# Performance work log

Hardware: AMD Instinct MI355X
Metric: run time of the kernel (lower is better)

Reference implementation:

```python
import jax, jax.numpy as jnp
import numpy as np

N_QUBITS = 16
NUM_CLASSES = 16
C64 = jnp.complex64


def rx_mat(theta):
    # RX(theta) = [[cos(t/2), -i sin(t/2)], [-i sin(t/2), cos(t/2)]]
    c = jnp.cos(theta / 2).astype(C64)
    s = jnp.sin(theta / 2).astype(C64)
    row0 = jnp.stack([c, -1j * s], axis=-1)
    row1 = jnp.stack([-1j * s, c], axis=-1)
    return jnp.stack([row0, row1], axis=-2)  # (..., 2, 2)


def rot_mat(phi, theta, omega):
    # PennyLane Rot = RZ(omega) RY(theta) RZ(phi)
    c = jnp.cos(theta / 2).astype(C64)
    s = jnp.sin(theta / 2).astype(C64)
    phi = phi.astype(C64)
    omega = omega.astype(C64)
    e_m = jnp.exp(-0.5j * (phi + omega))
    e_p = jnp.exp(0.5j * (phi + omega))
    e_d = jnp.exp(0.5j * (phi - omega))
    e_dm = jnp.exp(-0.5j * (phi - omega))
    return jnp.array([[e_m * c, -e_d * s], [e_dm * s, e_p * c]], dtype=C64)


def apply_1q(state, U, w):
    # state: (B, 2, ..., 2) with qubit w at axis 1+w; U: (2,2) or (B,2,2)
    s = jnp.moveaxis(state, 1 + w, -1)
    if U.ndim == 3:
        s = jnp.einsum('b...i,bji->b...j', s, U)
    else:
        s = jnp.einsum('...i,ji->...j', s, U)
    return jnp.moveaxis(s, -1, 1 + w)


def apply_crx(state, theta, ctrl, tgt):
    U = rx_mat(theta)  # (2, 2)
    s = jnp.moveaxis(state, (1 + ctrl, 1 + tgt), (-2, -1))
    s1 = jnp.einsum('...i,ji->...j', s[..., 1, :], U)
    s = jnp.stack([s[..., 0, :], s1], axis=-2)
    return jnp.moveaxis(s, (-2, -1), (1 + ctrl, 1 + tgt))


def circuit(feats, rot1, crx1, rot2, crx2):
    # feats: (B, 16) rotation angles (data re-uploading)
    B = feats.shape[0]
    state = jnp.zeros((B,) + (2,) * N_QUBITS, dtype=C64)
    state = state.at[(slice(None),) + (0,) * N_QUBITS].set(1.0)

    def layer(state, rot_w, crx_w):
        for i in range(N_QUBITS):
            state = apply_1q(state, rx_mat(feats[:, i]), i)  # batched RX
        for i in range(N_QUBITS):
            state = apply_1q(state, rot_mat(rot_w[i, 0], rot_w[i, 1], rot_w[i, 2]), i)
        for i in range(N_QUBITS):
            state = apply_crx(state, crx_w[i], i, (i + 1) % N_QUBITS)
        return state

    state = layer(state, rot1, crx1)
    state = layer(state, rot2, crx2)

    probs = (state.real ** 2 + state.imag ** 2)  # (B, 2, ..., 2) float32
    evs = []
    for i in range(N_QUBITS):
        p = jnp.moveaxis(probs, 1 + i, 1).reshape(B, 2, -1).sum(-1)
        evs.append(p[:, 0] - p[:, 1])  # <Z_i>
    return jnp.stack(evs, axis=1)  # (B, 16)


def adaptive_pool_441(x):
    # AdaptiveAvgPool3d((4,4,1)) with divisible dims -> block means
    B, C, D, H, W = x.shape
    x = x.reshape(B, C, 4, D // 4, 4, H // 4, 1, W)
    return x.mean(axis=(3, 5, 7))  # (B, C, 4, 4, 1)


def setup_inputs() -> dict:
    key = jax.random.key(0)
    ks = jax.random.split(key, 9)
    B = 128
    x = jax.random.normal(ks[0], (B, 2, 16, 64, 64), dtype=jnp.float32)
    compress_w = jax.random.normal(ks[1], (N_QUBITS, 32), jnp.float32) * 0.1
    compress_b = jax.random.normal(ks[2], (N_QUBITS,), jnp.float32) * 0.01
    rot1 = jax.random.normal(ks[3], (N_QUBITS, 3), jnp.float32) * 0.1
    crx1 = jax.random.normal(ks[4], (N_QUBITS,), jnp.float32) * 0.1
    rot2 = jax.random.normal(ks[5], (N_QUBITS, 3), jnp.float32) * 0.1
    crx2 = jax.random.normal(ks[6], (N_QUBITS,), jnp.float32) * 0.1
    fc_w = jax.random.normal(ks[7], (NUM_CLASSES, N_QUBITS), jnp.float32) * 0.1
    fc_b = jax.random.normal(ks[8], (NUM_CLASSES,), jnp.float32) * 0.01
    return {"x": x, "compress_w": compress_w, "compress_b": compress_b,
            "rot1": rot1, "crx1": crx1, "rot2": rot2, "crx2": crx2,
            "fc_w": fc_w, "fc_b": fc_b}


def reference(x, compress_w, compress_b, rot1, crx1, rot2, crx2, fc_w, fc_b):
    B = x.shape[0]
    p = adaptive_pool_441(x).reshape(B, -1)          # (B, 32)
    feats = p @ compress_w.T + compress_b            # (B, 16)
    q_out = circuit(feats, rot1, crx1, rot2, crx2)   # (B, 16)
    logits = q_out @ fc_w.T + fc_b                   # (B, 16)
    return jax.nn.log_softmax(logits, axis=1)
```

## Files before the change

### kernel.cpp

```cpp
#include <hip/hip_runtime.h>
#include <hip/hip_bf16.h>

typedef float f2 __attribute__((ext_vector_type(2)));

__device__ __forceinline__ f2 sgate(f2 a, int lane, int kt, int kc, const float* u) {
    f2 p;
    p.x = __shfl_xor(a.x, 1 << kt);
    p.y = __shfl_xor(a.y, 1 << kt);
    const float* uu = u + ((kc >= 0 && ((lane >> kc) & 1)) ? 8 : 0);
    int bit = (lane >> kt) & 1;
    float cAr = bit ? uu[6] : uu[0], cAi = bit ? uu[7] : uu[1];
    float cPr = bit ? uu[4] : uu[2], cPi = bit ? uu[5] : uu[3];
    f2 r;
    r.x = cAr * a.x - cAi * a.y + cPr * p.x - cPi * p.y;
    r.y = cAr * a.y + cAi * a.x + cPr * p.y + cPi * p.x;
    return r;
}

__device__ __forceinline__ f2 cmul(f2 A, f2 B) {
    return f2{A.x * B.x - A.y * B.y, A.x * B.y + A.y * B.x};
}
__device__ __forceinline__ f2 cmulc(f2 x, f2 y) {
    return f2{x.x * y.x + x.y * y.y, x.y * y.x - x.x * y.y};
}

__global__ __launch_bounds__(256) void qall2(const float* __restrict__ x,
                                             const float* __restrict__ cw,
                                             const float* __restrict__ cb,
                                             const float* __restrict__ rot1,
                                             const float* __restrict__ crx1,
                                             const float* __restrict__ rot2,
                                             const float* __restrict__ crx2,
                                             const float* __restrict__ fcw,
                                             const float* __restrict__ fcb,
                                             float* __restrict__ out) {
    __shared__ float pp[32];
    __shared__ float uM[32][16];
    __shared__ float cs15[4];
    __shared__ f2 ell[64];
    __shared__ f2 Rr[2][64];
    __shared__ f2 Wl[2][32];
    __shared__ f2 Btab[4][64];
    __shared__ f2 Ctab[8][32];
    __shared__ float Rtab[2][4][64];
    __shared__ float sH[2][6][32];
    __shared__ float sD[2][32];
    __shared__ float sE[2][32];
    __shared__ float redP[4][7];
    __shared__ float redQ[4][8];
    __shared__ float evf[16];
    __shared__ float lgf[16];
    int tid = threadIdx.x;
    int b = blockIdx.x;

    {
        int g = tid >> 3, sub = tid & 7;
        int c = g >> 4, dd = (g >> 2) & 3, hh = g & 3;
        const float4* xb = (const float4*)(x + (size_t)b * 131072)
                         + c * 16384 + dd * 4096 + hh * 256;
        float sum = 0.f;
        #pragma unroll
        for (int d = 0; d < 4; ++d) {
            const float4* ch = xb + d * 1024;
            #pragma unroll 8
            for (int i = 0; i < 32; ++i) {
                float4 v = ch[i * 8 + sub];
                sum += v.x + v.y + v.z + v.w;
            }
        }
        sum += __shfl_xor(sum, 1);
        sum += __shfl_xor(sum, 2);
        sum += __shfl_xor(sum, 4);
        if (sub == 0) pp[g] = sum * (1.0f / 4096.0f);
    }
    __syncthreads();

    if (tid < 32) {
        int q = tid & 15, l = tid >> 4;
        float f = cb[q];
        #pragma unroll
        for (int jj = 0; jj < 32; ++jj) f += pp[jj] * cw[q * 32 + jj];
        float cr = cosf(0.5f * f), sr = sinf(0.5f * f);
        const float* rw = (l == 0 ? rot1 : rot2) + q * 3;
        float phi = rw[0], th = rw[1], om = rw[2];
        float ct = cosf(0.5f * th), st = sinf(0.5f * th);
        float aa = 0.5f * (phi + om), dd = 0.5f * (phi - om);
        float ca = cosf(aa), sa = sinf(aa), cd = cosf(dd), sd = sinf(dd);
        float R00r =  ct * ca, R00i = -ct * sa;
        float R01r = -st * cd, R01i = -st * sd;
        float R10r =  st * cd, R10i = -st * sd;
        float R11r =  ct * ca, R11i =  ct * sa;
        float u0 = cr * R00r + sr * R01i;
        float u1 = cr * R00i - sr * R01r;
        float u2 = cr * R01r + sr * R00i;
        float u3 = cr * R01i - sr * R00r;
        float u4 = cr * R10r + sr * R11i;
        float u5 = cr * R10i - sr * R11r;
        float u6 = cr * R11r + sr * R10i;
        float u7 = cr * R11i - sr * R10r;
        float g[16];
        g[0] = u0; g[1] = u1; g[2] = u2; g[3] = u3;
        g[4] = u4; g[5] = u5; g[6] = u6; g[7] = u7;
        if (q >= 1) {
            float thc = (l == 0 ? crx1 : crx2)[q - 1];
            float c2 = cosf(0.5f * thc), s2 = sinf(0.5f * thc);
            g[8]  = c2*u0 + s2*u5;  g[9]  = c2*u1 - s2*u4;
            g[10] = c2*u2 + s2*u7;  g[11] = c2*u3 - s2*u6;
            g[12] = c2*u4 + s2*u1;  g[13] = c2*u5 - s2*u0;
            g[14] = c2*u6 + s2*u3;  g[15] = c2*u7 - s2*u2;
        } else {
            #pragma unroll
            for (int k = 0; k < 8; ++k) g[8 + k] = g[k];
        }
        float* s = uM[l * 16 + q];
        #pragma unroll
        for (int k = 0; k < 16; ++k) s[k] = g[k];
        if (q == 15) {
            float th2 = (l == 0 ? crx1 : crx2)[15];
            cs15[l * 2]     = cosf(0.5f * th2);
            cs15[l * 2 + 1] = sinf(0.5f * th2);
        }
    }
    __syncthreads();

    int wv = tid >> 6, lane = tid & 63;

    if (wv == 0) {
        f2 a = (lane == 0) ? f2{1.f, 0.f} : f2{0.f, 0.f};
        a = sgate(a, lane, 0, -1, uM[0]);
        #pragma unroll
        for (int q = 1; q <= 5; ++q) a = sgate(a, lane, q, q - 1, uM[q]);
        ell[lane] = a;
    } else if (wv <= 2) {
        int pidx = wv - 1;
        const float* m6 = uM[6] + pidx * 8;
        f2 a = f2{0.f, 0.f};
        if (lane == 0) a = f2{m6[0], m6[1]};
        if (lane == 1) a = f2{m6[4], m6[5]};
        #pragma unroll
        for (int q = 7; q <= 11; ++q) a = sgate(a, lane, q - 6, q - 7, uM[q]);
        Rr[pidx][lane] = a;
    } else {
        int j = lane >> 5, lm = lane & 31;
        f2 a = (lm == j) ? f2{1.f, 0.f} : f2{0.f, 0.f};
        #pragma unroll
        for (int q = 12; q <= 15; ++q) a = sgate(a, lane, q - 11, q - 12, uM[q]);
        Wl[j][lm] = a;
    }
    __syncthreads();

    {
        int c = wv >> 1, pb = wv & 1;
        f2 a = ell[lane];
        if (((lane >> 5) & 1) != pb) a = f2{0.f, 0.f};
        if (c) {
            f2 pr; pr.x = __shfl_xor(a.x, 1); pr.y = __shfl_xor(a.y, 1);
            f2 n = cs15[0] * a;
            n.x += cs15[1] * pr.y; n.y -= cs15[1] * pr.x;
            a = n;
        }
        a = sgate(a, lane, 0, -1, uM[16]);
        #pragma unroll
        for (int q = 1; q <= 5; ++q) a = sgate(a, lane, q, q - 1, uM[16 + q]);
        Btab[wv][lane] = a;
    }
    {
        int pidx = wv >> 1, p2 = wv & 1, j = lane >> 5, lm = lane & 31;
        f2 a = Rr[pidx][(j << 5) | lm];
        a = sgate(a, lane, 0, -1, uM[16 + 6] + p2 * 8);
        #pragma unroll
        for (int q = 7; q <= 10; ++q) a = sgate(a, lane, q - 6, q - 7, uM[16 + q]);
        Ctab[(pidx * 2 + j) * 2 + p2][lm] = a;
    }
    {
        int c = wv >> 1, bsel = wv & 1, j = lane >> 5, lm = lane & 31;
        f2 a = Wl[j][lm];
        if (((lm >> 4) & 1) != c) a = f2{0.f, 0.f};
        a = sgate(a, lane, 0, -1, uM[16 + 11] + bsel * 8);
        #pragma unroll
        for (int q = 12; q <= 15; ++q) a = sgate(a, lane, q - 11, q - 12, uM[16 + q]);
        Rtab[bsel][c * 2 + j][2 * lm]     = a.x;
        Rtab[bsel][c * 2 + j][2 * lm + 1] = a.y;
    }
    __syncthreads();

    if (tid < 192) {
        int bsel = tid / 96, rem = tid % 96, pt = rem >> 4, kk = rem & 15;
        int k = kk >> 2, k2 = kk & 3;
        float c15 = cs15[2], s15 = cs15[3];
        f2 Elo = f2{0.f, 0.f}, Ehi = f2{0.f, 0.f};
        #pragma unroll
        for (int m = 0; m < 32; ++m) {
            float rk = Rtab[bsel][k][2 * m],  ik = Rtab[bsel][k][2 * m + 1];
            float rp = Rtab[bsel][k2][2 * m], ip = Rtab[bsel][k2][2 * m + 1];
            float sg = (pt == 0) ? 1.f : (((m >> (pt - 1)) & 1) ? -1.f : 1.f);
            float wr = sg * (rk * rp + ik * ip);
            float wi = sg * (ik * rp - rk * ip);
            if (m < 16) { Elo.x += wr; Elo.y += wi; }
            else        { Ehi.x += wr; Ehi.y += wi; }
        }
        sH[bsel][pt][2 * kk]     = Elo.x + Ehi.x;
        sH[bsel][pt][2 * kk + 1] = Elo.y + Ehi.y;
        if (pt == 0) {
            float ccss = c15 * c15 - s15 * s15;
            sD[bsel][2 * kk]     = Elo.x + ccss * Ehi.x;
            sD[bsel][2 * kk + 1] = Elo.y + ccss * Ehi.y;
            float cs = c15 * s15;
            sE[bsel][2 * kk]     = cs * Ehi.x;
            sE[bsel][2 * kk + 1] = cs * Ehi.y;
        }
    }
    __syncthreads();

    int x0 = 2 * (tid & 31), x1 = x0 + 1;
    int x5 = (tid >> 4) & 1;

    f2 B0[2][2], B1[2][2];
    #pragma unroll
    for (int c = 0; c < 2; ++c)
        #pragma unroll
        for (int pq = 0; pq < 2; ++pq) {
            B0[c][pq] = Btab[c * 2 + pq][x0];
            B1[c][pq] = Btab[c * 2 + pq][x1];
        }

    float Pa = 0.f, P9 = 0.f, P10 = 0.f, Pd = 0.f;
    float S0 = 0.f, S1 = 0.f, S2 = 0.f, S3 = 0.f, S4 = 0.f;

    for (int part = 0; part < 4; ++part) {
        int bsel = part >> 1;
        int y = part * 8 + (tid >> 5);
        f2 Cv[2][2];
        #pragma unroll
        for (int pq = 0; pq < 2; ++pq)
            #pragma unroll
            for (int j = 0; j < 2; ++j)
                Cv[pq][j] = Ctab[(pq * 2 + j) * 2 + x5][y];

        f2 a[4], bb[4];
        #pragma unroll
        for (int c = 0; c < 2; ++c)
            #pragma unroll
            for (int j = 0; j < 2; ++j) {
                f2 s0 = cmul(B0[c][0], Cv[0][j]);
                f2 s1 = cmul(B0[c][1], Cv[1][j]);
                a[c * 2 + j] = f2{s0.x + s1.x, s0.y + s1.y};
                f2 t0 = cmul(B1[c][0], Cv[0][j]);
                f2 t1 = cmul(B1[c][1], Cv[1][j]);
                bb[c * 2 + j] = f2{t0.x + t1.x, t0.y + t1.y};
            }

        float sum_d[4], dif_d[4];
        #pragma unroll
        for (int k = 0; k < 4; ++k) {
            float pa = a[k].x * a[k].x + a[k].y * a[k].y;
            float pb = bb[k].x * bb[k].x + bb[k].y * bb[k].y;
            sum_d[k] = pa + pb;
            dif_d[k] = pa - pb;
        }
        f2 wS[6], wD[6];
        {
            int pi = 0;
            #pragma unroll
            for (int k = 0; k < 4; ++k)
                #pragma unroll
                for (int k2 = k + 1; k2 < 4; ++k2) {
                    f2 u = cmulc(a[k], a[k2]);
                    f2 v = cmulc(bb[k], bb[k2]);
                    wS[pi] = f2{u.x + v.x, u.y + v.y};
                    wD[pi] = f2{u.x - v.x, u.y - v.y};
                    ++pi;
                }
        }

        float F[6];
        #pragma unroll
        for (int pt = 0; pt < 6; ++pt) {
            const float* Hk = sH[bsel][pt];
            float f = 0.f;
            #pragma unroll
            for (int k = 0; k < 4; ++k) f += Hk[(k * 4 + k) * 2] * sum_d[k];
            int pi = 0;
            #pragma unroll
            for (int k = 0; k < 4; ++k)
                #pragma unroll
                for (int k2 = k + 1; k2 < 4; ++k2) {
                    float hr = Hk[(k * 4 + k2) * 2], hi = Hk[(k * 4 + k2) * 2 + 1];
                    f += 2.f * (hr * wS[pi].x - hi * wS[pi].y);
                    ++pi;
                }
            F[pt] = f;
        }
        float pd_i;
        {
            const float* Dk = sD[bsel];
            const float* Ek = sE[bsel];
            float f = 0.f;
            #pragma unroll
            for (int k = 0; k < 4; ++k) f += Dk[(k * 4 + k) * 2] * dif_d[k];
            int pi = 0;
            #pragma unroll
            for (int k = 0; k < 4; ++k)
                #pragma unroll
                for (int k2 = k + 1; k2 < 4; ++k2) {
                    float dr = Dk[(k * 4 + k2) * 2], di = Dk[(k * 4 + k2) * 2 + 1];
                    f += 2.f * (dr * wD[pi].x - di * wD[pi].y);
                    ++pi;
                }
            f2 z = f2{0.f, 0.f};
            #pragma unroll
            for (int k = 0; k < 4; ++k) {
                f2 v = f2{0.f, 0.f};
                #pragma unroll
                for (int k2 = 0; k2 < 4; ++k2) {
                    float er = Ek[(k * 4 + k2) * 2], ei = Ek[(k * 4 + k2) * 2 + 1];
                    v.x += er * bb[k2].x + ei * bb[k2].y;
                    v.y += ei * bb[k2].x - er * bb[k2].y;
                }
                z.x += a[k].x * v.x - a[k].y * v.y;
                z.y += a[k].x * v.y + a[k].y * v.x;
            }
            pd_i = f - 4.f * z.y;
        }

        Pa  += F[0];
        P9  += (part & 1) ? -F[0] : F[0];
        P10 += (part & 2) ? -F[0] : F[0];
        Pd  += pd_i;
        S0 += F[1]; S1 += F[2]; S2 += F[3]; S3 += F[4]; S4 += F[5];
    }

    #pragma unroll
    for (int o = 1; o < 64; o <<= 1) {
        float tP = __shfl_xor(Pa, o);
        Pa = (lane & o) ? (tP - Pa) : (Pa + tP);
        Pd  += __shfl_xor(Pd, o);
        P9  += __shfl_xor(P9, o);
        P10 += __shfl_xor(P10, o);
        S0  += __shfl_xor(S0, o);
        S1  += __shfl_xor(S1, o);
        S2  += __shfl_xor(S2, o);
        S3  += __shfl_xor(S3, o);
        S4  += __shfl_xor(S4, o);
    }
    if ((lane & (lane - 1)) == 0) {
        int slot = (lane == 0) ? 0 : (31 - __clz((unsigned)lane)) + 1;
        redP[wv][slot] = Pa;
    }
    if (lane == 0) {
        redQ[wv][0] = Pd;  redQ[wv][1] = P9;  redQ[wv][2] = P10;
        redQ[wv][3] = S0;  redQ[wv][4] = S1;  redQ[wv][5] = S2;
        redQ[wv][6] = S3;  redQ[wv][7] = S4;
    }
    __syncthreads();
    if (tid < 16) {
        int q = tid;
        float v;
        if (q == 0)      v = redQ[0][0] + redQ[1][0] + redQ[2][0] + redQ[3][0];
        else if (q < 7)  v = redP[0][q] + redP[1][q] + redP[2][q] + redP[3][q];
        else if (q == 7) v = redP[0][0] - redP[1][0] + redP[2][0] - redP[3][0];
        else if (q == 8) v = redP[0][0] + redP[1][0] - redP[2][0] - redP[3][0];
        else if (q == 9)  v = redQ[0][1] + redQ[1][1] + redQ[2][1] + redQ[3][1];
        else if (q == 10) v = redQ[0][2] + redQ[1][2] + redQ[2][2] + redQ[3][2];
        else              v = redQ[0][q-8] + redQ[1][q-8] + redQ[2][q-8] + redQ[3][q-8];
        evf[q] = v;
    }
    __syncthreads();

    if (tid < 16) {
        int c = tid;
        float v = fcb[c];
        #pragma unroll
        for (int q = 0; q < 16; ++q) v += evf[q] * fcw[c * 16 + q];
        lgf[c] = v;
    }
    __syncthreads();
    if (tid < 16) {
        float mx = -1e30f;
        #pragma unroll
        for (int c2 = 0; c2 < 16; ++c2) mx = fmaxf(mx, lgf[c2]);
        float se = 0.f;
        #pragma unroll
        for (int c2 = 0; c2 < 16; ++c2) se += expf(lgf[c2] - mx);
        out[b * 16 + tid] = lgf[tid] - (mx + logf(se));
    }
}

extern "C" void kernel_launch(void* const* d_in, const int* in_sizes, int n_in,
                              void* d_out, int out_size, void* d_ws, size_t ws_size,
                              hipStream_t stream) {
    const float* x    = (const float*)d_in[0];
    const float* cw   = (const float*)d_in[1];
    const float* cb   = (const float*)d_in[2];
    const float* rot1 = (const float*)d_in[3];
    const float* crx1 = (const float*)d_in[4];
    const float* rot2 = (const float*)d_in[5];
    const float* crx2 = (const float*)d_in[6];
    const float* fcw  = (const float*)d_in[7];
    const float* fcb  = (const float*)d_in[8];

    qall2<<<128, 256, 0, stream>>>(x, cw, cb, rot1, crx1, rot2, crx2,
                                   fcw, fcb, (float*)d_out);
}
```

Before: 27.84 us.

## Double block size to 512 threads, splitting pooling and state-part loop across waves

Launches 512 threads per block instead of 256. The input pooling now uses 16 threads per group, and the main per-part loop is split across two 256-thread groups (two parts each instead of four), with the cross-wave reduction redone over 8 waves and the P9/P10 sign combinations rebuilt from per-wave partials. The aim is more parallelism per block, since only 128 blocks run, to hide the latency of the memory-bound pooling and the serial compute loop. The cost is larger reductions and idle extra waves during the table-building phases, plus possible register pressure under the higher launch bound.

```diff
diff --git a/kernel.cpp b/kernel.cpp
--- a/kernel.cpp
+++ b/kernel.cpp
@@ -24,7 +24,7 @@
     return f2{x.x * y.x + x.y * y.y, x.y * y.x - x.x * y.y};
 }
 
-__global__ __launch_bounds__(256) void qall2(const float* __restrict__ x,
+__global__ __launch_bounds__(512) void qall2(const float* __restrict__ x,
                                              const float* __restrict__ cw,
                                              const float* __restrict__ cb,
                                              const float* __restrict__ rot1,
@@ -46,15 +46,15 @@
     __shared__ float sH[2][6][32];
     __shared__ float sD[2][32];
     __shared__ float sE[2][32];
-    __shared__ float redP[4][7];
-    __shared__ float redQ[4][8];
+    __shared__ float redP[8][7];
+    __shared__ float redQ[8][7];
     __shared__ float evf[16];
     __shared__ float lgf[16];
     int tid = threadIdx.x;
     int b = blockIdx.x;
 
     {
-        int g = tid >> 3, sub = tid & 7;
+        int g = tid >> 4, sub = tid & 15;
         int c = g >> 4, dd = (g >> 2) & 3, hh = g & 3;
         const float4* xb = (const float4*)(x + (size_t)b * 131072)
                          + c * 16384 + dd * 4096 + hh * 256;
@@ -63,14 +63,15 @@
         for (int d = 0; d < 4; ++d) {
             const float4* ch = xb + d * 1024;
             #pragma unroll 8
-            for (int i = 0; i < 32; ++i) {
-                float4 v = ch[i * 8 + sub];
+            for (int i = 0; i < 16; ++i) {
+                float4 v = ch[i * 16 + sub];
                 sum += v.x + v.y + v.z + v.w;
             }
         }
         sum += __shfl_xor(sum, 1);
         sum += __shfl_xor(sum, 2);
         sum += __shfl_xor(sum, 4);
+        sum += __shfl_xor(sum, 8);
         if (sub == 0) pp[g] = sum * (1.0f / 4096.0f);
     }
     __syncthreads();
@@ -140,7 +141,7 @@
         #pragma unroll
         for (int q = 7; q <= 11; ++q) a = sgate(a, lane, q - 6, q - 7, uM[q]);
         Rr[pidx][lane] = a;
-    } else {
+    } else if (wv == 3) {
         int j = lane >> 5, lm = lane & 31;
         f2 a = (lm == j) ? f2{1.f, 0.f} : f2{0.f, 0.f};
         #pragma unroll
@@ -149,38 +150,40 @@
     }
     __syncthreads();
 
-    {
-        int c = wv >> 1, pb = wv & 1;
-        f2 a = ell[lane];
-        if (((lane >> 5) & 1) != pb) a = f2{0.f, 0.f};
-        if (c) {
-            f2 pr; pr.x = __shfl_xor(a.x, 1); pr.y = __shfl_xor(a.y, 1);
-            f2 n = cs15[0] * a;
-            n.x += cs15[1] * pr.y; n.y -= cs15[1] * pr.x;
-            a = n;
-        }
-        a = sgate(a, lane, 0, -1, uM[16]);
-        #pragma unroll
-        for (int q = 1; q <= 5; ++q) a = sgate(a, lane, q, q - 1, uM[16 + q]);
-        Btab[wv][lane] = a;
-    }
-    {
-        int pidx = wv >> 1, p2 = wv & 1, j = lane >> 5, lm = lane & 31;
-        f2 a = Rr[pidx][(j << 5) | lm];
-        a = sgate(a, lane, 0, -1, uM[16 + 6] + p2 * 8);
-        #pragma unroll
-        for (int q = 7; q <= 10; ++q) a = sgate(a, lane, q - 6, q - 7, uM[16 + q]);
-        Ctab[(pidx * 2 + j) * 2 + p2][lm] = a;
-    }
-    {
-        int c = wv >> 1, bsel = wv & 1, j = lane >> 5, lm = lane & 31;
-        f2 a = Wl[j][lm];
-        if (((lm >> 4) & 1) != c) a = f2{0.f, 0.f};
-        a = sgate(a, lane, 0, -1, uM[16 + 11] + bsel * 8);
-        #pragma unroll
-        for (int q = 12; q <= 15; ++q) a = sgate(a, lane, q - 11, q - 12, uM[16 + q]);
-        Rtab[bsel][c * 2 + j][2 * lm]     = a.x;
-        Rtab[bsel][c * 2 + j][2 * lm + 1] = a.y;
+    if (wv < 4) {
+        {
+            int c = wv >> 1, pb = wv & 1;
+            f2 a = ell[lane];
+            if (((lane >> 5) & 1) != pb) a = f2{0.f, 0.f};
+            if (c) {
+                f2 pr; pr.x = __shfl_xor(a.x, 1); pr.y = __shfl_xor(a.y, 1);
+                f2 n = cs15[0] * a;
+                n.x += cs15[1] * pr.y; n.y -= cs15[1] * pr.x;
+                a = n;
+            }
+            a = sgate(a, lane, 0, -1, uM[16]);
+            #pragma unroll
+            for (int q = 1; q <= 5; ++q) a = sgate(a, lane, q, q - 1, uM[16 + q]);
+            Btab[wv][lane] = a;
+        }
+        {
+            int pidx = wv >> 1, p2 = wv & 1, j = lane >> 5, lm = lane & 31;
+            f2 a = Rr[pidx][(j << 5) | lm];
+            a = sgate(a, lane, 0, -1, uM[16 + 6] + p2 * 8);
+            #pragma unroll
+            for (int q = 7; q <= 10; ++q) a = sgate(a, lane, q - 6, q - 7, uM[16 + q]);
+            Ctab[(pidx * 2 + j) * 2 + p2][lm] = a;
+        }
+        {
+            int c = wv >> 1, bsel = wv & 1, j = lane >> 5, lm = lane & 31;
+            f2 a = Wl[j][lm];
+            if (((lm >> 4) & 1) != c) a = f2{0.f, 0.f};
+            a = sgate(a, lane, 0, -1, uM[16 + 11] + bsel * 8);
+            #pragma unroll
+            for (int q = 12; q <= 15; ++q) a = sgate(a, lane, q - 11, q - 12, uM[16 + q]);
+            Rtab[bsel][c * 2 + j][2 * lm]     = a.x;
+            Rtab[bsel][c * 2 + j][2 * lm + 1] = a.y;
+        }
     }
     __syncthreads();
 
@@ -212,8 +215,10 @@
     }
     __syncthreads();
 
-    int x0 = 2 * (tid & 31), x1 = x0 + 1;
-    int x5 = (tid >> 4) & 1;
+    int sub = tid & 255;
+    int grp = tid >> 8;
+    int x0 = 2 * (sub & 31), x1 = x0 + 1;
+    int x5 = (sub >> 4) & 1;
 
     f2 B0[2][2], B1[2][2];
     #pragma unroll
@@ -224,12 +229,14 @@
             B1[c][pq] = Btab[c * 2 + pq][x1];
         }
 
-    float Pa = 0.f, P9 = 0.f, P10 = 0.f, Pd = 0.f;
+    float Pa = 0.f, P9 = 0.f, Pd = 0.f;
     float S0 = 0.f, S1 = 0.f, S2 = 0.f, S3 = 0.f, S4 = 0.f;
 
-    for (int part = 0; part < 4; ++part) {
-        int bsel = part >> 1;
-        int y = part * 8 + (tid >> 5);
+    #pragma unroll
+    for (int pl = 0; pl < 2; ++pl) {
+        int part = grp * 2 + pl;
+        int bsel = grp;
+        int y = part * 8 + (sub >> 5);
         f2 Cv[2][2];
         #pragma unroll
         for (int pq = 0; pq < 2; ++pq)
@@ -323,10 +330,9 @@
             pd_i = f - 4.f * z.y;
         }
 
-        Pa  += F[0];
-        P9  += (part & 1) ? -F[0] : F[0];
-        P10 += (part & 2) ? -F[0] : F[0];
-        Pd  += pd_i;
+        Pa += F[0];
+        P9 += pl ? -F[0] : F[0];
+        Pd += pd_i;
         S0 += F[1]; S1 += F[2]; S2 += F[3]; S3 += F[4]; S4 += F[5];
     }
 
@@ -336,7 +342,6 @@
         Pa = (lane & o) ? (tP - Pa) : (Pa + tP);
         Pd  += __shfl_xor(Pd, o);
         P9  += __shfl_xor(P9, o);
-        P10 += __shfl_xor(P10, o);
         S0  += __shfl_xor(S0, o);
         S1  += __shfl_xor(S1, o);
         S2  += __shfl_xor(S2, o);
@@ -348,21 +353,36 @@
         redP[wv][slot] = Pa;
     }
     if (lane == 0) {
-        redQ[wv][0] = Pd;  redQ[wv][1] = P9;  redQ[wv][2] = P10;
-        redQ[wv][3] = S0;  redQ[wv][4] = S1;  redQ[wv][5] = S2;
-        redQ[wv][6] = S3;  redQ[wv][7] = S4;
+        redQ[wv][0] = Pd;  redQ[wv][1] = P9;
+        redQ[wv][2] = S0;  redQ[wv][3] = S1;  redQ[wv][4] = S2;
+        redQ[wv][5] = S3;  redQ[wv][6] = S4;
     }
     __syncthreads();
     if (tid < 16) {
         int q = tid;
-        float v;
-        if (q == 0)      v = redQ[0][0] + redQ[1][0] + redQ[2][0] + redQ[3][0];
-        else if (q < 7)  v = redP[0][q] + redP[1][q] + redP[2][q] + redP[3][q];
-        else if (q == 7) v = redP[0][0] - redP[1][0] + redP[2][0] - redP[3][0];
-        else if (q == 8) v = redP[0][0] + redP[1][0] - redP[2][0] - redP[3][0];
-        else if (q == 9)  v = redQ[0][1] + redQ[1][1] + redQ[2][1] + redQ[3][1];
-        else if (q == 10) v = redQ[0][2] + redQ[1][2] + redQ[2][2] + redQ[3][2];
-        else              v = redQ[0][q-8] + redQ[1][q-8] + redQ[2][q-8] + redQ[3][q-8];
+        float v = 0.f;
+        if (q == 0) {
+            #pragma unroll
+            for (int w = 0; w < 8; ++w) v += redQ[w][0];
+        } else if (q < 7) {
+            #pragma unroll
+            for (int w = 0; w < 8; ++w) v += redP[w][q];
+        } else if (q == 7) {
+            #pragma unroll
+            for (int w = 0; w < 8; ++w) v += (w & 1) ? -redP[w][0] : redP[w][0];
+        } else if (q == 8) {
+            #pragma unroll
+            for (int w = 0; w < 8; ++w) v += (w & 2) ? -redP[w][0] : redP[w][0];
+        } else if (q == 9) {
+            #pragma unroll
+            for (int w = 0; w < 8; ++w) v += redQ[w][1];
+        } else if (q == 10) {
+            #pragma unroll
+            for (int w = 0; w < 8; ++w) v += (w & 4) ? -redP[w][0] : redP[w][0];
+        } else {
+            #pragma unroll
+            for (int w = 0; w < 8; ++w) v += redQ[w][q - 9];
+        }
         evf[q] = v;
     }
     __syncthreads();
@@ -399,6 +419,6 @@
     const float* fcw  = (const float*)d_in[7];
     const float* fcb  = (const float*)d_in[8];
 
-    qall2<<<128, 256, 0, stream>>>(x, cw, cb, rot1, crx1, rot2, crx2,
+    qall2<<<128, 512, 0, stream>>>(x, cw, cb, rot1, crx1, rot2, crx2,
                                    fcw, fcb, (float*)d_out);
 }
```

Result: no change. 27.34 us (-1.8%).
